# Performance work log

Hardware: AMD Instinct MI355X
Metric: run time of the kernel (lower is better)

The kernel has to match this reference:

```python
import jax, jax.numpy as jnp
import numpy as np


def _find(parent, x):
    # chase parent pointers to the root (root = min-rank node of its component)
    return jax.lax.while_loop(lambda v: parent[v] != v, lambda v: parent[v], x)


def _pd0_single(fcol, src, dst):
    """0-dim persistence diagram for one filtration column.

    Semantics match TOGL.generate_persistence_diagram_dim0:
      - nodes are added in sorted order of fcol; birth(node) = its sorted rank
      - directed edge (u, v) merges components at step rank(v) iff rank(u) < rank(v)
      - elder rule: the component whose root has the larger rank dies
      - output row i = (birth=i, death) for the node of rank i (insertion order of
        the original dict is exactly rank order); death = inf for survivors.
    """
    n = fcol.shape[0]
    order = jnp.argsort(fcol)
    rank = jnp.zeros((n,), jnp.int32).at[order].set(jnp.arange(n, dtype=jnp.int32))
    a = rank[src]                      # rank-space endpoints
    b = rank[dst]
    valid = a < b                      # only edges whose source is already active fire
    w = jnp.where(valid, b, n)         # edge weight = step at which it fires
    perm = jnp.argsort(w)              # Kruskal order
    ea, eb, ev = a[perm], b[perm], valid[perm]

    def step(carry, e):
        parent, deaths = carry
        ia, ib, v = e
        ra = _find(parent, ia)
        rb = _find(parent, ib)
        merge = v & (ra != rb)
        elder = jnp.minimum(ra, rb)
        younger = jnp.maximum(ra, rb)
        deaths = deaths.at[younger].set(jnp.where(merge, ib.astype(deaths.dtype), deaths[younger]))
        parent = parent.at[younger].set(jnp.where(merge, elder, parent[younger]))
        # path compression at the two queried nodes
        parent = parent.at[ia].set(jnp.where(merge, elder, ra))
        parent = parent.at[ib].set(jnp.where(merge, elder, rb))
        return (parent, deaths), None

    parent0 = jnp.arange(n, dtype=jnp.int32)
    deaths0 = jnp.full((n,), jnp.inf, jnp.float32)
    (parent, deaths), _ = jax.lax.scan(step, (parent0, deaths0), (ea, eb, ev))
    births = jnp.arange(n, dtype=jnp.float32)
    return jnp.stack([births, deaths], axis=1)  # (n_nodes, 2)


def setup_inputs() -> dict:
    key = jax.random.key(0)
    k = jax.random.split(key, 6)
    N, F, H, NF, E = 20000, 1024, 2048, 4, 160000
    X = jax.random.normal(k[0], (N, F), jnp.float32)
    edge_index = jax.random.randint(k[1], (2, E), 0, N, jnp.int64)
    W1 = jax.random.normal(k[2], (F, H), jnp.float32) / np.sqrt(F)
    b1 = jax.random.normal(k[3], (H,), jnp.float32) * 0.01
    W2 = jax.random.normal(k[4], (H, NF), jnp.float32) / np.sqrt(H)
    b2 = jax.random.normal(k[5], (NF,), jnp.float32) * 0.01
    return {"X": X, "edge_index": edge_index, "W1": W1, "b1": b1, "W2": W2, "b2": b2}


def reference(X, edge_index, W1, b1, W2, b2):
    # filter_graph: Linear -> ReLU -> Linear
    filt = jnp.maximum(X @ W1 + b1, 0.0) @ W2 + b2            # (N, n_filtrations)
    src = edge_index[0].astype(jnp.int32)
    dst = edge_index[1].astype(jnp.int32)
    diagrams = jax.vmap(_pd0_single, in_axes=(1, None, None))(filt, src, dst)  # (NF, N, 2)
    return filt, diagrams
```

## Files before the change

kernel.cpp:

```cpp
#include <hip/hip_runtime.h>

typedef unsigned long long u64;
typedef unsigned int u32;
typedef unsigned short ushort_t;
typedef __attribute__((ext_vector_type(8))) short short8;
typedef __attribute__((ext_vector_type(4))) float fx4;

#define F_DIM 1024
#define H_DIM 2048
#define NFOUT 4
#define WS_W1T_OFF (1u << 20)

__device__ __forceinline__ ushort_t f2bf(float x)
{
    union { float f; u32 u; } c; c.f = x;
    u32 b = c.u;
    u32 r = b + 0x7FFFu + ((b >> 16) & 1u);
    return (ushort_t)(r >> 16);
}
__device__ __forceinline__ float bf2f(ushort_t h)
{
    union { u32 u; float f; } c; c.u = ((u32)h) << 16;
    return c.f;
}
__device__ __forceinline__ void split3(float x, ushort_t& u0, ushort_t& u1, ushort_t& u2)
{
    u0 = f2bf(x);
    float r1 = x - bf2f(u0);
    u1 = f2bf(r1);
    float r2 = r1 - bf2f(u1);
    u2 = f2bf(r2);
}

__global__ __launch_bounds__(256)
void k_w1split(const float* __restrict__ W1, ushort_t* __restrict__ w1t)
{
    __shared__ __align__(16) ushort_t LT[3][64][72];
    const int t = threadIdx.x;
    const int bk = blockIdx.x >> 5;
    const int bh = blockIdx.x & 31;
    const int k0 = bk * 64, h0 = bh * 64;
    const int kk = t >> 4, hb = (t & 15) * 4;
    #pragma unroll
    for (int j = 0; j < 4; j++) {
        int row = kk + j * 16;
        float4 v = *(const float4*)(W1 + (size_t)(k0 + row) * H_DIM + h0 + hb);
        float xs[4] = { v.x, v.y, v.z, v.w };
        #pragma unroll
        for (int c = 0; c < 4; c++) {
            ushort_t u0, u1, u2;
            split3(xs[c], u0, u1, u2);
            LT[0][hb + c][row] = u0;
            LT[1][hb + c][row] = u1;
            LT[2][hb + c][row] = u2;
        }
    }
    __syncthreads();
    const int hl = t >> 2, sg = t & 3;
    #pragma unroll
    for (int p = 0; p < 3; p++)
        #pragma unroll
        for (int q = 0; q < 2; q++) {
            int ks = sg * 16 + q * 8;
            *(short8*)(w1t + (size_t)p * (H_DIM * (size_t)F_DIM)
                       + (size_t)(h0 + hl) * F_DIM + k0 + ks) =
                *(const short8*)&LT[p][hl][ks];
        }
}

__device__ __forceinline__ fx4 mfma16(short8 a, short8 b, fx4 c)
{
    return __builtin_amdgcn_mfma_f32_16x16x32_bf16(a, b, c, 0, 0, 0);
}

__global__ __launch_bounds__(256, 2)
void k_filt_mfma(const float* __restrict__ X, const ushort_t* __restrict__ w1t,
                 const float* __restrict__ b1, const float* __restrict__ W2,
                 const float* __restrict__ b2, float* __restrict__ out, int N)
{
    __shared__ __align__(16) ushort_t Ap[3 * 64 * 64];
    __shared__ __align__(16) ushort_t Bp[3 * 128 * 64];
    __shared__ __align__(16) float4 W2s[128];
    float* hid  = (float*)Bp;
    float* part = (float*)Ap;
    char* Ac = (char*)Ap;
    char* Bc = (char*)Bp;

    const int t = threadIdx.x;
    const int lane = t & 63;
    const int w = t >> 6;
    const int wr = (w & 1) * 32;
    const int wc = (w >> 1) * 64;
    const int r0 = blockIdx.x * 64;
    const int l15 = lane & 15, l4 = lane >> 4;

    const int arow = t >> 2;
    const int ak16 = (t & 3) * 16;
    const int brow = t >> 1;
    const int bhalf = (t & 1) * 64;

    float pacc0 = 0.f, pacc1 = 0.f, pacc2 = 0.f, pacc3 = 0.f;

    for (int hc = 0; hc < H_DIM / 128; hc++) {
        fx4 acc[2][4];
        #pragma unroll
        for (int i = 0; i < 2; i++)
            #pragma unroll
            for (int j = 0; j < 4; j++) acc[i][j] = (fx4)(0.f);

        if (t < 128) W2s[t] = *(const float4*)(W2 + ((size_t)hc * 128 + t) * NFOUT);

        for (int kc = 0; kc < F_DIM / 64; kc++) {
            __syncthreads();
            {
                int rg = r0 + arow;
                float xv[16];
                if (rg < N) {
                    #pragma unroll
                    for (int q = 0; q < 4; q++) {
                        float4 v = *(const float4*)(X + (size_t)rg * F_DIM + kc * 64 + ak16 + q * 4);
                        xv[q * 4 + 0] = v.x; xv[q * 4 + 1] = v.y;
                        xv[q * 4 + 2] = v.z; xv[q * 4 + 3] = v.w;
                    }
                } else {
                    #pragma unroll
                    for (int q = 0; q < 16; q++) xv[q] = 0.f;
                }
                ushort_t u[3][16];
                #pragma unroll
                for (int q = 0; q < 16; q++) split3(xv[q], u[0][q], u[1][q], u[2][q]);
                const int swz = (arow & 7) << 4;
                #pragma unroll
                for (int p = 0; p < 3; p++)
                    #pragma unroll
                    for (int hs = 0; hs < 2; hs++) {
                        short8 pk;
                        #pragma unroll
                        for (int i = 0; i < 8; i++) pk[i] = (short)u[p][hs * 8 + i];
                        *(short8*)(Ac + p * 8192 + arow * 128 + ((ak16 * 2 + hs * 16) ^ swz)) = pk;
                    }
            }
            {
                const int swz = (brow & 7) << 4;
                const size_t gb = ((size_t)(hc * 128 + brow)) * F_DIM + kc * 64;
                #pragma unroll
                for (int p = 0; p < 3; p++)
                    #pragma unroll
                    for (int q = 0; q < 4; q++) {
                        short8 v = *(const short8*)(w1t + (size_t)p * (H_DIM * (size_t)F_DIM)
                                                    + gb + (bhalf + q * 16) / 2);
                        *(short8*)(Bc + p * 16384 + brow * 128 + ((bhalf + q * 16) ^ swz)) = v;
                    }
            }
            __syncthreads();
            #pragma unroll
            for (int sub = 0; sub < 2; sub++) {
                const int kb = sub * 64 + l4 * 16;
                short8 a[2][3], b[4][3];
                #pragma unroll
                for (int rr = 0; rr < 2; rr++) {
                    int row = wr + rr * 16 + l15;
                    int sw = (row & 7) << 4;
                    #pragma unroll
                    for (int p = 0; p < 3; p++)
                        a[rr][p] = *(const short8*)(Ac + p * 8192 + row * 128 + (kb ^ sw));
                }
                #pragma unroll
                for (int cf = 0; cf < 4; cf++) {
                    int hrow = wc + cf * 16 + l15;
                    int sw = (hrow & 7) << 4;
                    #pragma unroll
                    for (int p = 0; p < 3; p++)
                        b[cf][p] = *(const short8*)(Bc + p * 16384 + hrow * 128 + (kb ^ sw));
                }
                #pragma unroll
                for (int rr = 0; rr < 2; rr++)
                    #pragma unroll
                    for (int cf = 0; cf < 4; cf++) {
                        fx4 c = acc[rr][cf];
                        c = mfma16(a[rr][0], b[cf][0], c);
                        c = mfma16(a[rr][0], b[cf][1], c);
                        c = mfma16(a[rr][1], b[cf][0], c);
                        c = mfma16(a[rr][0], b[cf][2], c);
                        c = mfma16(a[rr][1], b[cf][1], c);
                        c = mfma16(a[rr][2], b[cf][0], c);
                        acc[rr][cf] = c;
                    }
            }
        }
        __syncthreads();
        #pragma unroll
        for (int rr = 0; rr < 2; rr++)
            #pragma unroll
            for (int cf = 0; cf < 4; cf++) {
                int hl = wc + cf * 16 + l15;
                float b1v = b1[hc * 128 + hl];
                #pragma unroll
                for (int g = 0; g < 4; g++) {
                    int rl = wr + rr * 16 + l4 * 4 + g;
                    hid[rl * 132 + hl] = fmaxf(acc[rr][cf][g] + b1v, 0.f);
                }
            }
        __syncthreads();
        {
            const int row = t >> 2, hl0 = t & 3;
            #pragma unroll 8
            for (int j = 0; j < 32; j++) {
                int h = hl0 + j * 4;
                float hv = hid[row * 132 + h];
                float4 wv = W2s[h];
                pacc0 = fmaf(hv, wv.x, pacc0);
                pacc1 = fmaf(hv, wv.y, pacc1);
                pacc2 = fmaf(hv, wv.z, pacc2);
                pacc3 = fmaf(hv, wv.w, pacc3);
            }
        }
    }
    __syncthreads();
    {
        const int row = t >> 2, hl = t & 3;
        part[row * 16 + hl * 4 + 0] = pacc0;
        part[row * 16 + hl * 4 + 1] = pacc1;
        part[row * 16 + hl * 4 + 2] = pacc2;
        part[row * 16 + hl * 4 + 3] = pacc3;
    }
    __syncthreads();
    {
        const int row = t >> 2, nf = t & 3;
        float s = ((part[row * 16 + 0 + nf] + part[row * 16 + 4 + nf])
                   + part[row * 16 + 8 + nf]) + part[row * 16 + 12 + nf];
        int rg = r0 + row;
        if (rg < N) out[(size_t)rg * NFOUT + nf] = s + b2[nf];
    }
}

#define BM 64
#define BH 64
#define KCH 64
#define LROW 68

__global__ __launch_bounds__(256, 2)
void k_filt(const float* __restrict__ X, const float* __restrict__ W1,
            const float* __restrict__ b1, const float* __restrict__ W2,
            const float* __restrict__ b2, float* __restrict__ out, int N)
{
    __shared__ float Xs[KCH * LROW];
    __shared__ float Ws[KCH * LROW];
    __shared__ float W2s[BH * NFOUT];
    const int t = threadIdx.x;
    const int r0 = blockIdx.x * BM;
    const int tr = t >> 4, tc = t & 15;
    const int orow = t >> 2, onf = t & 3;
    float fchain = 0.0f;
    for (int hc = 0; hc < H_DIM; hc += BH) {
        float acc[4][4];
        #pragma unroll
        for (int i = 0; i < 4; i++)
            #pragma unroll
            for (int j = 0; j < 4; j++) acc[i][j] = 0.0f;
        for (int kc = 0; kc < F_DIM; kc += KCH) {
            {
                const int rowq = t >> 4, kkq = t & 15;
                float xv[4][4];
                #pragma unroll
                for (int j = 0; j < 4; j++) {
                    int r = r0 + rowq * 4 + j;
                    float4 v = (r < N) ? *(const float4*)(X + (size_t)r * F_DIM + kc + kkq * 4)
                                       : make_float4(0.f, 0.f, 0.f, 0.f);
                    xv[j][0] = v.x; xv[j][1] = v.y; xv[j][2] = v.z; xv[j][3] = v.w;
                }
                #pragma unroll
                for (int j = 0; j < 4; j++)
                    *(float4*)&Xs[(kkq * 4 + j) * LROW + rowq * 4] =
                        make_float4(xv[0][j], xv[1][j], xv[2][j], xv[3][j]);
            }
            {
                const int hq = t & 15;
                #pragma unroll
                for (int q = 0; q < 4; q++) {
                    int kk = (t >> 4) + q * 16;
                    *(float4*)&Ws[kk * LROW + hq * 4] =
                        *(const float4*)(W1 + (size_t)(kc + kk) * H_DIM + hc + hq * 4);
                }
            }
            __syncthreads();
            #pragma unroll 8
            for (int kk = 0; kk < KCH; kk++) {
                float4 xv = *(float4*)&Xs[kk * LROW + tr * 4];
                float4 wv = *(float4*)&Ws[kk * LROW + tc * 4];
                acc[0][0] = fmaf(xv.x, wv.x, acc[0][0]); acc[0][1] = fmaf(xv.x, wv.y, acc[0][1]);
                acc[0][2] = fmaf(xv.x, wv.z, acc[0][2]); acc[0][3] = fmaf(xv.x, wv.w, acc[0][3]);
                acc[1][0] = fmaf(xv.y, wv.x, acc[1][0]); acc[1][1] = fmaf(xv.y, wv.y, acc[1][1]);
                acc[1][2] = fmaf(xv.y, wv.z, acc[1][2]); acc[1][3] = fmaf(xv.y, wv.w, acc[1][3]);
                acc[2][0] = fmaf(xv.z, wv.x, acc[2][0]); acc[2][1] = fmaf(xv.z, wv.y, acc[2][1]);
                acc[2][2] = fmaf(xv.z, wv.z, acc[2][2]); acc[2][3] = fmaf(xv.z, wv.w, acc[2][3]);
                acc[3][0] = fmaf(xv.w, wv.x, acc[3][0]); acc[3][1] = fmaf(xv.w, wv.y, acc[3][1]);
                acc[3][2] = fmaf(xv.w, wv.z, acc[3][2]); acc[3][3] = fmaf(xv.w, wv.w, acc[3][3]);
            }
            __syncthreads();
        }
        {
            float4 bv = *(const float4*)(b1 + hc + tc * 4);
            #pragma unroll
            for (int i = 0; i < 4; i++) {
                float4 hv;
                hv.x = fmaxf(acc[i][0] + bv.x, 0.f);
                hv.y = fmaxf(acc[i][1] + bv.y, 0.f);
                hv.z = fmaxf(acc[i][2] + bv.z, 0.f);
                hv.w = fmaxf(acc[i][3] + bv.w, 0.f);
                *(float4*)&Ws[(tr * 4 + i) * LROW + tc * 4] = hv;
            }
            if (t < BH)
                *(float4*)&W2s[t * 4] = *(const float4*)(W2 + (size_t)(hc + t) * NFOUT);
        }
        __syncthreads();
        #pragma unroll 16
        for (int hh = 0; hh < BH; hh++)
            fchain = fmaf(Ws[orow * LROW + hh], W2s[hh * 4 + onf], fchain);
        __syncthreads();
    }
    {
        int r = r0 + orow;
        if (r < N) out[(size_t)r * NFOUT + onf] = fchain + b2[onf];
    }
}

__global__ void k_prep(u32* __restrict__ rank, int N)
{
    int g = blockIdx.x * blockDim.x + threadIdx.x;
    if (g < 4 * N) rank[g] = 0u;
}

#define JTILE 2048

__global__ __launch_bounds__(256)
void k_rank(const float* __restrict__ filt, u32* __restrict__ rank,
            int N, int nchunk)
{
    __shared__ float4 lds[JTILE];
    const int chunk = blockIdx.x % nchunk;
    const int jslice = blockIdx.x / nchunk;
    const int jt = jslice * JTILE;
    const int i = chunk * 256 + threadIdx.x;
    const bool iok = i < N;
    float4 vi = iok ? *(const float4*)(filt + (size_t)i * 4)
                    : make_float4(0.f, 0.f, 0.f, 0.f);
    for (int s = 0; s < JTILE; s += 256) {
        int j = jt + s + threadIdx.x;
        lds[s + threadIdx.x] = (j < N)
            ? *(const float4*)(filt + (size_t)j * 4)
            : make_float4(INFINITY, INFINITY, INFINITY, INFINITY);
    }
    __syncthreads();
    int c0 = 0, c1 = 0, c2 = 0, c3 = 0;
    #pragma unroll 4
    for (int jj = 0; jj < JTILE; jj++) {
        float4 vj = lds[jj];
        int j = jt + jj;
        bool jlt = j < i;
        c0 += (vj.x < vi.x) || (vj.x == vi.x && jlt);
        c1 += (vj.y < vi.y) || (vj.y == vi.y && jlt);
        c2 += (vj.z < vi.z) || (vj.z == vi.z && jlt);
        c3 += (vj.w < vi.w) || (vj.w == vi.w && jlt);
    }
    if (iok) {
        atomicAdd(&rank[0 * N + i], (u32)c0);
        atomicAdd(&rank[1 * N + i], (u32)c1);
        atomicAdd(&rank[2 * N + i], (u32)c2);
        atomicAdd(&rank[3 * N + i], (u32)c3);
    }
}

__device__ __forceinline__ u32 lds_aload(u32* p)
{
    return __hip_atomic_load(p, __ATOMIC_RELAXED, __HIP_MEMORY_SCOPE_WORKGROUP);
}

__device__ __forceinline__ u32 rep_walk32(u32* S, u32 u, u32 t, u32& sv_out)
{
    u32 sv = lds_aload(&S[u]);
    while ((sv >> 16) <= t) {
        u = sv & 0xFFFFu;
        sv = lds_aload(&S[u]);
    }
    sv_out = sv;
    return u;
}

__device__ void do_merge32(u32* S, u32 u, u32 v, u32 t)
{
    for (int guard = 0; guard < (1 << 22); guard++) {
        u32 svu, svv;
        u = rep_walk32(S, u, t, svu);
        v = rep_walk32(S, v, t, svv);
        if (u == v) return;
        if (u < v) { u32 tm = u; u = v; v = tm; u32 ts = svu; svu = svv; svv = ts; }
        u32 s = svu >> 16;
        if (s <= t) continue;
        u32 des = (t << 16) | v;
        u32 old = atomicCAS(&S[u], svu, des);
        if (old == svu) {
            if (s == 0xFFFFu) return;
            u = v; v = old & 0xFFFFu;
            t = s;
        }
    }
}

__global__ __launch_bounds__(1024, 1)
void k_merge4(const int* __restrict__ eidx, const u32* __restrict__ rank,
              float* __restrict__ dg, int N, int E)
{
    extern __shared__ u32 S[];
    const int f = blockIdx.x;
    const u32* rk = rank + (size_t)f * N;

    for (int u = threadIdx.x; u < N; u += blockDim.x)
        S[u] = (0xFFFFu << 16) | (u32)u;
    __syncthreads();

    for (int e = threadIdx.x; e < E; e += blockDim.x) {
        u32 a = rk[eidx[e]];
        u32 b = rk[eidx[E + e]];
        if (a < b) do_merge32(S, a, b, b);
    }
    __syncthreads();

    for (int r = threadIdx.x; r < N; r += blockDim.x) {
        u32 s = S[r] >> 16;
        float death = (s == 0xFFFFu) ? 3.0e38f : (float)s;
        dg[(size_t)f * N * 2 + (size_t)r * 2 + 0] = (float)r;
        dg[(size_t)f * N * 2 + (size_t)r * 2 + 1] = death;
    }
}

extern "C" void kernel_launch(void* const* d_in, const int* in_sizes, int n_in,
                              void* d_out, int out_size, void* d_ws, size_t ws_size,
                              hipStream_t stream)
{
    const float* X  = (const float*)d_in[0];
    const int*   EI = (const int*)d_in[1];
    const float* W1 = (const float*)d_in[2];
    const float* b1 = (const float*)d_in[3];
    const float* W2 = (const float*)d_in[4];
    const float* b2 = (const float*)d_in[5];
    const int N = in_sizes[0] / F_DIM;
    const int E = in_sizes[1] / 2;

    float* out = (float*)d_out;
    float* dg  = out + (size_t)N * NFOUT;
    u32* rank  = (u32*)d_ws;

    static bool attr_set = false;
    if (!attr_set) {
        (void)hipFuncSetAttribute((const void*)k_merge4,
                                  hipFuncAttributeMaxDynamicSharedMemorySize,
                                  160 * 1024);
        attr_set = true;
    }

    k_prep<<<(4 * N + 255) / 256, 256, 0, stream>>>(rank, N);

    const size_t w1t_need = (size_t)WS_W1T_OFF + 3ull * H_DIM * F_DIM * 2;
    if (ws_size >= w1t_need) {
        ushort_t* w1t = (ushort_t*)((char*)d_ws + WS_W1T_OFF);
        k_w1split<<<512, 256, 0, stream>>>(W1, w1t);
        k_filt_mfma<<<(N + 63) / 64, 256, 0, stream>>>(X, w1t, b1, W2, b2, out, N);
    } else {
        k_filt<<<(N + BM - 1) / BM, 256, 0, stream>>>(X, W1, b1, W2, b2, out, N);
    }

    const int nchunk = (N + 255) / 256;
    const int njt    = (N + JTILE - 1) / JTILE;
    k_rank<<<nchunk * njt, 256, 0, stream>>>(out, rank, N, nchunk);
    k_merge4<<<4, 1024, (size_t)N * sizeof(u32), stream>>>(EI, rank, dg, N, E);
}
```

Baseline: 1.720 ms.

## Widen MFMA filter GEMM tile to 256 hidden cols with register-prefetched global loads

The bf16x3 MFMA filter kernel now uses 512 threads and a 64x256 output tile, double-buffering the next K-chunk of X and split W1 in registers while the current chunk is computed from LDS. The nested hc/kc loops are flattened into one loop, and the second linear layer is split across waves by output feature and hidden half. The intent is to hide global load latency and halve how often X is re-read and re-split per hidden chunk. In exchange it uses much more LDS through dynamic shared memory and more registers, which may lower occupancy.

Result: slower. 1.820 ms (+5.8%).

```diff
diff --git a/kernel.cpp b/kernel.cpp
--- a/kernel.cpp
+++ b/kernel.cpp
@@ -73,18 +73,22 @@
     return __builtin_amdgcn_mfma_f32_16x16x32_bf16(a, b, c, 0, 0, 0);
 }
 
-__global__ __launch_bounds__(256, 2)
+#define AP_BYTES (3 * 64 * 128)
+#define BP_BYTES (3 * 256 * 128)
+#define SM_BYTES (AP_BYTES + BP_BYTES + 256 * 4 * 4)
+#define HPITCH 261
+
+__global__ __launch_bounds__(512, 2)
 void k_filt_mfma(const float* __restrict__ X, const ushort_t* __restrict__ w1t,
                  const float* __restrict__ b1, const float* __restrict__ W2,
                  const float* __restrict__ b2, float* __restrict__ out, int N)
 {
-    __shared__ __align__(16) ushort_t Ap[3 * 64 * 64];
-    __shared__ __align__(16) ushort_t Bp[3 * 128 * 64];
-    __shared__ __align__(16) float4 W2s[128];
-    float* hid  = (float*)Bp;
-    float* part = (float*)Ap;
-    char* Ac = (char*)Ap;
-    char* Bc = (char*)Bp;
+    extern __shared__ char smem[];
+    char* Ac = smem;
+    char* Bc = smem + AP_BYTES;
+    float* W2s = (float*)(smem + AP_BYTES + BP_BYTES);
+    float* hid = (float*)Bc;
+    float* part = (float*)Ac;
 
     const int t = threadIdx.x;
     const int lane = t & 63;
@@ -94,142 +98,154 @@
     const int r0 = blockIdx.x * 64;
     const int l15 = lane & 15, l4 = lane >> 4;
 
-    const int arow = t >> 2;
-    const int ak16 = (t & 3) * 16;
+    const int arow = t >> 3;
+    const int ak8  = (t & 7) * 8;
+    const bool arow_ok = (r0 + arow) < N;
     const int brow = t >> 1;
-    const int bhalf = (t & 1) * 64;
-
-    float pacc0 = 0.f, pacc1 = 0.f, pacc2 = 0.f, pacc3 = 0.f;
-
-    for (int hc = 0; hc < H_DIM / 128; hc++) {
-        fx4 acc[2][4];
-        #pragma unroll
-        for (int i = 0; i < 2; i++)
-            #pragma unroll
-            for (int j = 0; j < 4; j++) acc[i][j] = (fx4)(0.f);
-
-        if (t < 128) W2s[t] = *(const float4*)(W2 + ((size_t)hc * 128 + t) * NFOUT);
-
-        for (int kc = 0; kc < F_DIM / 64; kc++) {
+    const int bseg = (t & 1) * 64;
+
+    const int g2row = lane;
+    const int g2nf  = w & 3;
+    const int g2seg = w >> 2;
+
+    float Afl[8];
+    short8 Bv[12];
+    fx4 acc[2][4];
+    float pacc = 0.f;
+    #pragma unroll
+    for (int i = 0; i < 2; i++)
+        #pragma unroll
+        for (int j = 0; j < 4; j++) acc[i][j] = (fx4)(0.f);
+
+    {
+        if (arow_ok) {
+            float4 v0 = *(const float4*)(X + (size_t)(r0 + arow) * F_DIM + ak8);
+            float4 v1 = *(const float4*)(X + (size_t)(r0 + arow) * F_DIM + ak8 + 4);
+            Afl[0] = v0.x; Afl[1] = v0.y; Afl[2] = v0.z; Afl[3] = v0.w;
+            Afl[4] = v1.x; Afl[5] = v1.y; Afl[6] = v1.z; Afl[7] = v1.w;
+        } else {
+            #pragma unroll
+            for (int j = 0; j < 8; j++) Afl[j] = 0.f;
+        }
+        #pragma unroll
+        for (int p = 0; p < 3; p++)
+            #pragma unroll
+            for (int q = 0; q < 4; q++)
+                Bv[p * 4 + q] = *(const short8*)(w1t + (size_t)p * (H_DIM * (size_t)F_DIM)
+                                 + (size_t)brow * F_DIM + (bseg + q * 16) / 2);
+    }
+
+    for (int it = 0; it < 128; ++it) {
+        const int hc = it >> 4, kc = it & 15;
+
+        ushort_t s0[8], s1[8], s2[8];
+        #pragma unroll
+        for (int j = 0; j < 8; j++) split3(Afl[j], s0[j], s1[j], s2[j]);
+        short8 Au0, Au1, Au2;
+        #pragma unroll
+        for (int j = 0; j < 8; j++) { Au0[j] = (short)s0[j]; Au1[j] = (short)s1[j]; Au2[j] = (short)s2[j]; }
+
+        __syncthreads();
+
+        {
+            const int aswz = (arow & 7) << 4;
+            const int abyte = (ak8 * 2);
+            *(short8*)(Ac + 0 * 8192 + arow * 128 + (abyte ^ aswz)) = Au0;
+            *(short8*)(Ac + 1 * 8192 + arow * 128 + (abyte ^ aswz)) = Au1;
+            *(short8*)(Ac + 2 * 8192 + arow * 128 + (abyte ^ aswz)) = Au2;
+            const int bswz = (brow & 7) << 4;
+            #pragma unroll
+            for (int p = 0; p < 3; p++)
+                #pragma unroll
+                for (int q = 0; q < 4; q++)
+                    *(short8*)(Bc + p * 32768 + brow * 128 + ((bseg + q * 16) ^ bswz)) = Bv[p * 4 + q];
+            if (kc == 0 && t < 256)
+                *(float4*)&W2s[t * 4] = *(const float4*)(W2 + ((size_t)hc * 256 + t) * NFOUT);
+        }
+
+        if (it + 1 < 128) {
+            const int hn = (it + 1) >> 4, kn = (it + 1) & 15;
+            if (arow_ok) {
+                float4 v0 = *(const float4*)(X + (size_t)(r0 + arow) * F_DIM + kn * 64 + ak8);
+                float4 v1 = *(const float4*)(X + (size_t)(r0 + arow) * F_DIM + kn * 64 + ak8 + 4);
+                Afl[0] = v0.x; Afl[1] = v0.y; Afl[2] = v0.z; Afl[3] = v0.w;
+                Afl[4] = v1.x; Afl[5] = v1.y; Afl[6] = v1.z; Afl[7] = v1.w;
+            }
+            #pragma unroll
+            for (int p = 0; p < 3; p++)
+                #pragma unroll
+                for (int q = 0; q < 4; q++)
+                    Bv[p * 4 + q] = *(const short8*)(w1t + (size_t)p * (H_DIM * (size_t)F_DIM)
+                                     + (size_t)(hn * 256 + brow) * F_DIM + kn * 64 + (bseg + q * 16) / 2);
+        }
+
+        __syncthreads();
+
+        #pragma unroll
+        for (int sub = 0; sub < 2; ++sub) {
+            const int kb = sub * 64 + l4 * 16;
+            const int sw = (l15 & 7) << 4;
+            short8 a[2][3];
+            #pragma unroll
+            for (int rr = 0; rr < 2; ++rr) {
+                const int row = wr + rr * 16 + l15;
+                #pragma unroll
+                for (int p = 0; p < 3; p++)
+                    a[rr][p] = *(const short8*)(Ac + p * 8192 + row * 128 + (kb ^ sw));
+            }
+            #pragma unroll
+            for (int cf = 0; cf < 4; ++cf) {
+                const int hrow = wc + cf * 16 + l15;
+                short8 bb0 = *(const short8*)(Bc + 0 * 32768 + hrow * 128 + (kb ^ sw));
+                short8 bb1 = *(const short8*)(Bc + 1 * 32768 + hrow * 128 + (kb ^ sw));
+                short8 bb2 = *(const short8*)(Bc + 2 * 32768 + hrow * 128 + (kb ^ sw));
+                #pragma unroll
+                for (int rr = 0; rr < 2; ++rr) {
+                    fx4 c = acc[rr][cf];
+                    c = mfma16(a[rr][0], bb0, c);
+                    c = mfma16(a[rr][0], bb1, c);
+                    c = mfma16(a[rr][1], bb0, c);
+                    c = mfma16(a[rr][0], bb2, c);
+                    c = mfma16(a[rr][1], bb1, c);
+                    c = mfma16(a[rr][2], bb0, c);
+                    acc[rr][cf] = c;
+                }
+            }
+        }
+
+        if (kc == 15) {
+            __syncthreads();
+            #pragma unroll
+            for (int rr = 0; rr < 2; ++rr)
+                #pragma unroll
+                for (int cf = 0; cf < 4; ++cf) {
+                    const int hl = wc + cf * 16 + l15;
+                    const float bias1 = b1[hc * 256 + hl];
+                    #pragma unroll
+                    for (int g = 0; g < 4; g++) {
+                        const int rl = wr + rr * 16 + l4 * 4 + g;
+                        hid[rl * HPITCH + hl] = fmaxf(acc[rr][cf][g] + bias1, 0.f);
+                    }
+                    acc[rr][cf] = (fx4)(0.f);
+                }
             __syncthreads();
             {
-                int rg = r0 + arow;
-                float xv[16];
-                if (rg < N) {
-                    #pragma unroll
-                    for (int q = 0; q < 4; q++) {
-                        float4 v = *(const float4*)(X + (size_t)rg * F_DIM + kc * 64 + ak16 + q * 4);
-                        xv[q * 4 + 0] = v.x; xv[q * 4 + 1] = v.y;
-                        xv[q * 4 + 2] = v.z; xv[q * 4 + 3] = v.w;
-                    }
-                } else {
-                    #pragma unroll
-                    for (int q = 0; q < 16; q++) xv[q] = 0.f;
-                }
-                ushort_t u[3][16];
-                #pragma unroll
-                for (int q = 0; q < 16; q++) split3(xv[q], u[0][q], u[1][q], u[2][q]);
-                const int swz = (arow & 7) << 4;
-                #pragma unroll
-                for (int p = 0; p < 3; p++)
-                    #pragma unroll
-                    for (int hs = 0; hs < 2; hs++) {
-                        short8 pk;
-                        #pragma unroll
-                        for (int i = 0; i < 8; i++) pk[i] = (short)u[p][hs * 8 + i];
-                        *(short8*)(Ac + p * 8192 + arow * 128 + ((ak16 * 2 + hs * 16) ^ swz)) = pk;
-                    }
-            }
-            {
-                const int swz = (brow & 7) << 4;
-                const size_t gb = ((size_t)(hc * 128 + brow)) * F_DIM + kc * 64;
-                #pragma unroll
-                for (int p = 0; p < 3; p++)
-                    #pragma unroll
-                    for (int q = 0; q < 4; q++) {
-                        short8 v = *(const short8*)(w1t + (size_t)p * (H_DIM * (size_t)F_DIM)
-                                                    + gb + (bhalf + q * 16) / 2);
-                        *(short8*)(Bc + p * 16384 + brow * 128 + ((bhalf + q * 16) ^ swz)) = v;
-                    }
-            }
-            __syncthreads();
-            #pragma unroll
-            for (int sub = 0; sub < 2; sub++) {
-                const int kb = sub * 64 + l4 * 16;
-                short8 a[2][3], b[4][3];
-                #pragma unroll
-                for (int rr = 0; rr < 2; rr++) {
-                    int row = wr + rr * 16 + l15;
-                    int sw = (row & 7) << 4;
-                    #pragma unroll
-                    for (int p = 0; p < 3; p++)
-                        a[rr][p] = *(const short8*)(Ac + p * 8192 + row * 128 + (kb ^ sw));
-                }
-                #pragma unroll
-                for (int cf = 0; cf < 4; cf++) {
-                    int hrow = wc + cf * 16 + l15;
-                    int sw = (hrow & 7) << 4;
-                    #pragma unroll
-                    for (int p = 0; p < 3; p++)
-                        b[cf][p] = *(const short8*)(Bc + p * 16384 + hrow * 128 + (kb ^ sw));
-                }
-                #pragma unroll
-                for (int rr = 0; rr < 2; rr++)
-                    #pragma unroll
-                    for (int cf = 0; cf < 4; cf++) {
-                        fx4 c = acc[rr][cf];
-                        c = mfma16(a[rr][0], b[cf][0], c);
-                        c = mfma16(a[rr][0], b[cf][1], c);
-                        c = mfma16(a[rr][1], b[cf][0], c);
-                        c = mfma16(a[rr][0], b[cf][2], c);
-                        c = mfma16(a[rr][1], b[cf][1], c);
-                        c = mfma16(a[rr][2], b[cf][0], c);
-                        acc[rr][cf] = c;
-                    }
-            }
-        }
-        __syncthreads();
-        #pragma unroll
-        for (int rr = 0; rr < 2; rr++)
-            #pragma unroll
-            for (int cf = 0; cf < 4; cf++) {
-                int hl = wc + cf * 16 + l15;
-                float b1v = b1[hc * 128 + hl];
-                #pragma unroll
-                for (int g = 0; g < 4; g++) {
-                    int rl = wr + rr * 16 + l4 * 4 + g;
-                    hid[rl * 132 + hl] = fmaxf(acc[rr][cf][g] + b1v, 0.f);
-                }
-            }
-        __syncthreads();
-        {
-            const int row = t >> 2, hl0 = t & 3;
-            #pragma unroll 8
-            for (int j = 0; j < 32; j++) {
-                int h = hl0 + j * 4;
-                float hv = hid[row * 132 + h];
-                float4 wv = W2s[h];
-                pacc0 = fmaf(hv, wv.x, pacc0);
-                pacc1 = fmaf(hv, wv.y, pacc1);
-                pacc2 = fmaf(hv, wv.z, pacc2);
-                pacc3 = fmaf(hv, wv.w, pacc3);
-            }
-        }
-    }
-    __syncthreads();
-    {
-        const int row = t >> 2, hl = t & 3;
-        part[row * 16 + hl * 4 + 0] = pacc0;
-        part[row * 16 + hl * 4 + 1] = pacc1;
-        part[row * 16 + hl * 4 + 2] = pacc2;
-        part[row * 16 + hl * 4 + 3] = pacc3;
-    }
-    __syncthreads();
-    {
+                const float* hp = hid + g2row * HPITCH + g2seg * 128;
+                const int hb = g2seg * 128;
+                #pragma unroll 16
+                for (int j = 0; j < 128; j++)
+                    pacc = fmaf(hp[j], W2s[(hb + j) * 4 + g2nf], pacc);
+            }
+        }
+    }
+
+    __syncthreads();
+    part[g2row * 8 + g2nf * 2 + g2seg] = pacc;
+    __syncthreads();
+    if (t < 256) {
         const int row = t >> 2, nf = t & 3;
-        float s = ((part[row * 16 + 0 + nf] + part[row * 16 + 4 + nf])
-                   + part[row * 16 + 8 + nf]) + part[row * 16 + 12 + nf];
-        int rg = r0 + row;
+        const float s = part[row * 8 + nf * 2 + 0] + part[row * 8 + nf * 2 + 1];
+        const int rg = r0 + row;
         if (rg < N) out[(size_t)rg * NFOUT + nf] = s + b2[nf];
     }
 }
@@ -456,6 +472,9 @@
         (void)hipFuncSetAttribute((const void*)k_merge4,
                                   hipFuncAttributeMaxDynamicSharedMemorySize,
                                   160 * 1024);
+        (void)hipFuncSetAttribute((const void*)k_filt_mfma,
+                                  hipFuncAttributeMaxDynamicSharedMemorySize,
+                                  160 * 1024);
         attr_set = true;
     }
 
@@ -465,7 +484,7 @@
     if (ws_size >= w1t_need) {
         ushort_t* w1t = (ushort_t*)((char*)d_ws + WS_W1T_OFF);
         k_w1split<<<512, 256, 0, stream>>>(W1, w1t);
-        k_filt_mfma<<<(N + 63) / 64, 256, 0, stream>>>(X, w1t, b1, W2, b2, out, N);
+        k_filt_mfma<<<(N + 63) / 64, 512, SM_BYTES, stream>>>(X, w1t, b1, W2, b2, out, N);
     } else {
         k_filt<<<(N + BM - 1) / BM, 256, 0, stream>>>(X, W1, b1, W2, b2, out, N);
     }
```
